# Optimization experiments

Hardware: AMD Instinct MI355X
Metric: run time of the kernel (lower is better)

The kernel has to match this reference:

```python
import jax, jax.numpy as jnp
import numpy as np

N_NODES = 50000
N_EDGES = 1600000
IN_F = 256
OUT_F = 128
ALPHA = 0.2  # LeakyReLU negative slope
EPS = 1e-9


def setup_inputs() -> dict:
    key = jax.random.key(0)
    k1, k2, k3, k4 = jax.random.split(key, 4)
    x = jax.random.normal(k1, (N_NODES, IN_F), dtype=jnp.float32)
    edge_index = jax.random.randint(k2, (2, N_EDGES), 0, N_NODES, dtype=jnp.int64)
    # xavier_uniform-ish scale for params
    W = jax.random.normal(k3, (IN_F, OUT_F), dtype=jnp.float32) * (1.414 / np.sqrt(IN_F + OUT_F))
    a = jax.random.normal(k4, (1, 2 * OUT_F), dtype=jnp.float32) * (1.414 / np.sqrt(1 + 2 * OUT_F))
    return {"x": x, "edge_index": edge_index, "W": W, "a": a}


def reference(x, edge_index, W, a):
    N = x.shape[0]
    F = W.shape[1]
    h = x @ W                                  # [N, F]
    src = edge_index[0]                        # row indices (aggregation target)
    dst = edge_index[1]                        # col indices (neighbor source)
    a_src = a[0, :F]                           # split a.mm(cat(h_src, h_dst).T)
    a_dst = a[0, F:]
    score = h[src] @ a_src + h[dst] @ a_dst    # [E]
    e = jnp.exp(-jax.nn.leaky_relu(score, negative_slope=ALPHA))  # [E]
    # e_rowsum = A @ ones : sum of edge values per row
    rowsum = jax.ops.segment_sum(e, src, num_segments=N)          # [N]
    # h_prime = A @ h : weighted neighbor aggregation per row
    agg = jax.ops.segment_sum(e[:, None] * h[dst], src, num_segments=N)  # [N, F]
    h_prime = agg / (rowsum[:, None] + EPS)
    return jax.nn.elu(h_prime)  # concat=True -> elu
```

## Files before the change

kernel.cpp:

```cpp
#include <hip/hip_runtime.h>
#include <hip/hip_bf16.h>
#include <math.h>

#define N_NODES 50000
#define N_EDGES 1600000
#define IN_F 256
#define OUT_F 128
#define ALPHA 0.2f
#define EPS 1e-9f

#define NPB 32
#define BINS 1563
#define SUBCAP 1536
#define MAXDEG 128
#define PTILE 8192
#define PGRID ((N_EDGES + PTILE - 1) / PTILE)

typedef __attribute__((ext_vector_type(8))) short short8v;
typedef __attribute__((ext_vector_type(4))) float f32x4;

__device__ __forceinline__ unsigned short bf16r(float f) {
  unsigned u = __float_as_uint(f);
  u = (u + 0x7FFFu + ((u >> 16) & 1u)) >> 16;
  return (unsigned short)u;
}

__global__ __launch_bounds__(256) void wcvt_k(const float* __restrict__ W,
                                              unsigned short* __restrict__ Wt) {
  int col = blockIdx.x;
  int k = threadIdx.x;
  Wt[col * IN_F + k] = bf16r(W[(size_t)k * OUT_F + col]);
}

__global__ __launch_bounds__(256) void gemm_mfma(const float* __restrict__ x,
                                                 const unsigned short* __restrict__ Wt,
                                                 const float* __restrict__ a,
                                                 unsigned short* __restrict__ hbs,
                                                 float* __restrict__ s1,
                                                 float* __restrict__ s2) {
  __shared__ float s1p[128], s2p[128];
  const int t = threadIdx.x;
  const int lane = t & 63;
  const int wv = t >> 6;
  const int row0 = blockIdx.x * 128;
  const int wcol0 = wv * 32;
  const int lrow = lane & 15;
  const int lk = (lane >> 4) * 8;

  for (int i = t; i < 128; i += 256) { s1p[i] = 0.f; s2p[i] = 0.f; }

  short8v b[2][8];
#pragma unroll
  for (int cg = 0; cg < 2; ++cg) {
    int col = wcol0 + cg * 16 + lrow;
#pragma unroll
    for (int ks = 0; ks < 8; ++ks)
      b[cg][ks] = *reinterpret_cast<const short8v*>(&Wt[col * IN_F + ks * 32 + lk]);
  }
  const float a1 = a[wcol0 + lrow];
  const float a1b = a[wcol0 + 16 + lrow];
  const float a2 = a[128 + wcol0 + lrow];
  const float a2b = a[128 + wcol0 + 16 + lrow];
  __syncthreads();

  for (int rg = 0; rg < 8; ++rg) {
    int row = row0 + rg * 16 + lrow;
    int rowc = row < N_NODES ? row : N_NODES - 1;
    const float* xr = &x[(size_t)rowc * IN_F];
    short8v av[8];
#pragma unroll
    for (int ks = 0; ks < 8; ++ks) {
      float4 u = *reinterpret_cast<const float4*>(&xr[ks * 32 + lk]);
      float4 v = *reinterpret_cast<const float4*>(&xr[ks * 32 + lk + 4]);
      short8v w;
      w[0] = (short)bf16r(u.x); w[1] = (short)bf16r(u.y);
      w[2] = (short)bf16r(u.z); w[3] = (short)bf16r(u.w);
      w[4] = (short)bf16r(v.x); w[5] = (short)bf16r(v.y);
      w[6] = (short)bf16r(v.z); w[7] = (short)bf16r(v.w);
      av[ks] = w;
    }
    f32x4 acc0 = {0.f, 0.f, 0.f, 0.f};
    f32x4 acc1 = {0.f, 0.f, 0.f, 0.f};
#pragma unroll
    for (int ks = 0; ks < 8; ++ks) {
      acc0 = __builtin_amdgcn_mfma_f32_16x16x32_bf16(av[ks], b[0][ks], acc0, 0, 0, 0);
      acc1 = __builtin_amdgcn_mfma_f32_16x16x32_bf16(av[ks], b[1][ks], acc1, 0, 0, 0);
    }
    int srow0 = row0 + rg * 16 + (lane >> 4) * 4;
#pragma unroll
    for (int r = 0; r < 4; ++r) {
      int srow = srow0 + r;
      if (srow < N_NODES) {
        hbs[(size_t)srow * OUT_F + wcol0 + lrow] = bf16r(acc0[r]);
        hbs[(size_t)srow * OUT_F + wcol0 + 16 + lrow] = bf16r(acc1[r]);
      }
      float p1 = acc0[r] * a1 + acc1[r] * a1b;
      float p2 = acc0[r] * a2 + acc1[r] * a2b;
#pragma unroll
      for (int m = 8; m >= 1; m >>= 1) {
        p1 += __shfl_xor(p1, m, 64);
        p2 += __shfl_xor(p2, m, 64);
      }
      if (lrow == 0) {
        int lr = rg * 16 + (lane >> 4) * 4 + r;
        atomicAdd(&s1p[lr], p1);
        atomicAdd(&s2p[lr], p2);
      }
    }
  }
  __syncthreads();
  for (int i = t; i < 128; i += 256) {
    int g = row0 + i;
    if (g < N_NODES) { s1[g] = s1p[i]; s2[g] = s2p[i]; }
  }
}

__device__ __forceinline__ int load_idx(const int* __restrict__ ei32, int isI64,
                                        long long pos) {
  if (isI64) return (int)(reinterpret_cast<const long long*>(ei32)[pos]);
  return ei32[pos];
}

__global__ __launch_bounds__(512) void part_k(const int* __restrict__ ei,
                                              unsigned* __restrict__ bins,
                                              int* __restrict__ bincur) {
  __shared__ int hist[BINS], cur[BINS], gbase[BINS];
  __shared__ int sf64;
  const int t = threadIdx.x;
  if (t < 64) {
    int nz = 0;
#pragma unroll
    for (int j = 0; j < 4; ++j) nz |= ei[2 * (t + j * 64) + 1];
    unsigned long long any = __ballot(nz != 0);
    if (t == 0) sf64 = (any == 0ull) ? 1 : 0;
  }
  for (int i = t; i < BINS; i += 512) hist[i] = 0;
  __syncthreads();
  const int f64 = sf64;
  const int base = blockIdx.x * PTILE;
  unsigned rec[16];
#pragma unroll
  for (int j = 0; j < 16; ++j) {
    int e = base + j * 512 + t;
    if (e < N_EDGES) {
      unsigned s = (unsigned)load_idx(ei, f64, e);
      unsigned d = (unsigned)load_idx(ei, f64, (long long)N_EDGES + e);
      rec[j] = (s << 16) | d;
      atomicAdd(&hist[s >> 5], 1);
    } else rec[j] = 0xFFFFFFFFu;
  }
  __syncthreads();
  for (int i = t; i < BINS; i += 512) {
    gbase[i] = hist[i] ? atomicAdd(&bincur[i], hist[i]) : 0;
    cur[i] = 0;
  }
  __syncthreads();
#pragma unroll
  for (int j = 0; j < 16; ++j) {
    if (rec[j] != 0xFFFFFFFFu) {
      int bb = rec[j] >> 21;
      int pos = atomicAdd(&cur[bb], 1);
      int o = gbase[bb] + pos;
      if (o < SUBCAP) bins[(size_t)bb * SUBCAP + o] = rec[j];
    }
  }
}

__global__ __launch_bounds__(512) void aggc_k(const unsigned* __restrict__ bins,
                                              const int* __restrict__ bincur,
                                              const float* __restrict__ s1,
                                              const float* __restrict__ s2,
                                              const unsigned* __restrict__ hb,
                                              float* __restrict__ out) {
  __shared__ unsigned sorted[SUBCAP];
  __shared__ uint2 ebuf[8][MAXDEG];
  __shared__ int hist[NPB], cur[NPB], rowptr[NPB + 1];
  const int t = threadIdx.x;
  const int b = blockIdx.x;
  const int lo = b * NPB;
  const int n_b = min(bincur[b], SUBCAP);
  const unsigned* bp = bins + (size_t)b * SUBCAP;

  if (t < NPB) hist[t] = 0;
  __syncthreads();
  unsigned rec[3];
#pragma unroll
  for (int r = 0; r < 3; ++r) {
    int i = t + r * 512;
    rec[r] = 0xFFFFFFFFu;
    if (i < n_b) {
      rec[r] = bp[i];
      atomicAdd(&hist[(rec[r] >> 16) & (NPB - 1)], 1);
    }
  }
  __syncthreads();
  if (t < NPB) {
    int c = hist[t];
    int incl = c;
#pragma unroll
    for (int off = 1; off < NPB; off <<= 1) {
      int v = __shfl_up(incl, off, 64);
      if (t >= off) incl += v;
    }
    rowptr[t + 1] = incl;
    cur[t] = incl - c;
    if (t == 0) rowptr[0] = 0;
  }
  __syncthreads();
#pragma unroll
  for (int r = 0; r < 3; ++r) {
    if (rec[r] != 0xFFFFFFFFu) {
      int sl = (rec[r] >> 16) & (NPB - 1);
      int pos = atomicAdd(&cur[sl], 1);
      sorted[pos] = rec[r] & 0xFFFFu;
    }
  }
  __syncthreads();

  const int wv = t >> 6, lane = t & 63;
  for (int i = 0; i < 4; ++i) {
    int nl = wv * 4 + i;
    int g = lo + nl;
    if (g >= N_NODES) continue;
    int rp = rowptr[nl];
    int cn = min(rowptr[nl + 1] - rp, MAXDEG);
    float s1u = s1[g];
    float rsl = 0.f;
    for (int j = lane; j < cn; j += 64) {
      unsigned d = sorted[rp + j];
      float sc = s1u + s2[d];
      float w = __expf(-fmaxf(sc, ALPHA * sc));
      ebuf[wv][j] = make_uint2(d << 6, __float_as_uint(w));
      rsl += w;
    }
#pragma unroll
    for (int m = 32; m >= 1; m >>= 1) rsl += __shfl_xor(rsl, m, 64);
    float accx = 0.f, accy = 0.f;
    int j = 0;
    for (; j + 7 < cn; j += 8) {
      uint4 e0 = *reinterpret_cast<const uint4*>(&ebuf[wv][j]);
      uint4 e1 = *reinterpret_cast<const uint4*>(&ebuf[wv][j + 2]);
      uint4 e2 = *reinterpret_cast<const uint4*>(&ebuf[wv][j + 4]);
      uint4 e3 = *reinterpret_cast<const uint4*>(&ebuf[wv][j + 6]);
      unsigned v0 = hb[e0.x | lane];
      unsigned v1 = hb[e0.z | lane];
      unsigned v2 = hb[e1.x | lane];
      unsigned v3 = hb[e1.z | lane];
      unsigned v4 = hb[e2.x | lane];
      unsigned v5 = hb[e2.z | lane];
      unsigned v6 = hb[e3.x | lane];
      unsigned v7 = hb[e3.z | lane];
      float w0 = __uint_as_float(e0.y), w1 = __uint_as_float(e0.w);
      float w2 = __uint_as_float(e1.y), w3 = __uint_as_float(e1.w);
      float w4 = __uint_as_float(e2.y), w5 = __uint_as_float(e2.w);
      float w6 = __uint_as_float(e3.y), w7 = __uint_as_float(e3.w);
      accx = fmaf(w0, __uint_as_float(v0 << 16), accx);
      accy = fmaf(w0, __uint_as_float(v0 & 0xFFFF0000u), accy);
      accx = fmaf(w1, __uint_as_float(v1 << 16), accx);
      accy = fmaf(w1, __uint_as_float(v1 & 0xFFFF0000u), accy);
      accx = fmaf(w2, __uint_as_float(v2 << 16), accx);
      accy = fmaf(w2, __uint_as_float(v2 & 0xFFFF0000u), accy);
      accx = fmaf(w3, __uint_as_float(v3 << 16), accx);
      accy = fmaf(w3, __uint_as_float(v3 & 0xFFFF0000u), accy);
      accx = fmaf(w4, __uint_as_float(v4 << 16), accx);
      accy = fmaf(w4, __uint_as_float(v4 & 0xFFFF0000u), accy);
      accx = fmaf(w5, __uint_as_float(v5 << 16), accx);
      accy = fmaf(w5, __uint_as_float(v5 & 0xFFFF0000u), accy);
      accx = fmaf(w6, __uint_as_float(v6 << 16), accx);
      accy = fmaf(w6, __uint_as_float(v6 & 0xFFFF0000u), accy);
      accx = fmaf(w7, __uint_as_float(v7 << 16), accx);
      accy = fmaf(w7, __uint_as_float(v7 & 0xFFFF0000u), accy);
    }
    for (; j < cn; ++j) {
      uint2 e = ebuf[wv][j];
      unsigned v0 = hb[e.x | lane];
      float w0 = __uint_as_float(e.y);
      accx = fmaf(w0, __uint_as_float(v0 << 16), accx);
      accy = fmaf(w0, __uint_as_float(v0 & 0xFFFF0000u), accy);
    }
    float inv = 1.0f / (rsl + EPS);
    float px = accx * inv, py = accy * inv;
    px = px > 0.f ? px : expm1f(px);
    py = py > 0.f ? py : expm1f(py);
    float2 o = {px, py};
    *reinterpret_cast<float2*>(&out[(size_t)g * OUT_F + 2 * lane]) = o;
  }
}

extern "C" void kernel_launch(void* const* d_in, const int* in_sizes, int n_in,
                              void* d_out, int out_size, void* d_ws, size_t ws_size,
                              hipStream_t stream) {
  const float* x = (const float*)d_in[0];
  const int* ei = (const int*)d_in[1];
  const float* W = (const float*)d_in[2];
  const float* a = (const float*)d_in[3];
  float* out = (float*)d_out;

  unsigned* hb = (unsigned*)d_ws;
  float* s1 = (float*)(hb + (size_t)N_NODES * 64);
  float* s2 = s1 + N_NODES;
  int* bincur = (int*)(s2 + N_NODES);
  unsigned* bins = (unsigned*)(bincur + BINS);
  unsigned short* Wt = (unsigned short*)(bins + (size_t)BINS * SUBCAP);

  hipMemsetAsync(bincur, 0, (size_t)BINS * sizeof(int), stream);

  wcvt_k<<<OUT_F, IN_F, 0, stream>>>(W, Wt);
  gemm_mfma<<<(N_NODES + 127) / 128, 256, 0, stream>>>(x, Wt, a, (unsigned short*)hb, s1, s2);
  part_k<<<PGRID, 512, 0, stream>>>(ei, bins, bincur);
  aggc_k<<<BINS, 512, 0, stream>>>(bins, bincur, s1, s2, hb, out);
}
```

Before: 128.9 us.

## Use buffer loads for gather, cheaper bf16 packing, larger partition tiles

The neighbor-feature gather in the aggregation kernel now goes through raw buffer loads with byte offsets when the builtin is available, falling back to plain pointer loads otherwise. The fp32-to-bf16 packing in the GEMM uses a simpler round-half-up pack of two values per word instead of per-element round-to-nearest-even. The partition kernel handles twice as many edges per block, halving the grid, and the in-LDS sorted neighbor list shrinks to 16-bit entries. Together these aim to cut address arithmetic, ALU work, launch blocks and LDS footprint, at the cost of slightly different rounding, more registers in the partition kernel and fewer partition blocks in flight.

```diff
diff --git a/kernel.cpp b/kernel.cpp
--- a/kernel.cpp
+++ b/kernel.cpp
@@ -13,16 +13,28 @@
 #define BINS 1563
 #define SUBCAP 1536
 #define MAXDEG 128
-#define PTILE 8192
+#define PTILE 16384
 #define PGRID ((N_EDGES + PTILE - 1) / PTILE)
 
 typedef __attribute__((ext_vector_type(8))) short short8v;
 typedef __attribute__((ext_vector_type(4))) float f32x4;
+
+#if defined(__has_builtin)
+#if __has_builtin(__builtin_amdgcn_raw_buffer_load_b32) && __has_builtin(__builtin_amdgcn_make_buffer_rsrc)
+#define HAVE_RAWBUF 1
+#endif
+#endif
 
 __device__ __forceinline__ unsigned short bf16r(float f) {
   unsigned u = __float_as_uint(f);
   u = (u + 0x7FFFu + ((u >> 16) & 1u)) >> 16;
   return (unsigned short)u;
+}
+
+__device__ __forceinline__ unsigned pk2(float a, float b) {
+  unsigned ua = (__float_as_uint(a) + 0x8000u) >> 16;
+  unsigned ub = (__float_as_uint(b) + 0x8000u) & 0xFFFF0000u;
+  return ua | ub;
 }
 
 __global__ __launch_bounds__(256) void wcvt_k(const float* __restrict__ W,
@@ -72,12 +84,12 @@
     for (int ks = 0; ks < 8; ++ks) {
       float4 u = *reinterpret_cast<const float4*>(&xr[ks * 32 + lk]);
       float4 v = *reinterpret_cast<const float4*>(&xr[ks * 32 + lk + 4]);
-      short8v w;
-      w[0] = (short)bf16r(u.x); w[1] = (short)bf16r(u.y);
-      w[2] = (short)bf16r(u.z); w[3] = (short)bf16r(u.w);
-      w[4] = (short)bf16r(v.x); w[5] = (short)bf16r(v.y);
-      w[6] = (short)bf16r(v.z); w[7] = (short)bf16r(v.w);
-      av[ks] = w;
+      union { short8v s; unsigned u[4]; } cv;
+      cv.u[0] = pk2(u.x, u.y);
+      cv.u[1] = pk2(u.z, u.w);
+      cv.u[2] = pk2(v.x, v.y);
+      cv.u[3] = pk2(v.z, v.w);
+      av[ks] = cv.s;
     }
     f32x4 acc0 = {0.f, 0.f, 0.f, 0.f};
     f32x4 acc1 = {0.f, 0.f, 0.f, 0.f};
@@ -138,9 +150,9 @@
   __syncthreads();
   const int f64 = sf64;
   const int base = blockIdx.x * PTILE;
-  unsigned rec[16];
-#pragma unroll
-  for (int j = 0; j < 16; ++j) {
+  unsigned rec[32];
+#pragma unroll
+  for (int j = 0; j < 32; ++j) {
     int e = base + j * 512 + t;
     if (e < N_EDGES) {
       unsigned s = (unsigned)load_idx(ei, f64, e);
@@ -156,7 +168,7 @@
   }
   __syncthreads();
 #pragma unroll
-  for (int j = 0; j < 16; ++j) {
+  for (int j = 0; j < 32; ++j) {
     if (rec[j] != 0xFFFFFFFFu) {
       int bb = rec[j] >> 21;
       int pos = atomicAdd(&cur[bb], 1);
@@ -172,7 +184,7 @@
                                               const float* __restrict__ s2,
                                               const unsigned* __restrict__ hb,
                                               float* __restrict__ out) {
-  __shared__ unsigned sorted[SUBCAP];
+  __shared__ unsigned short sorted[SUBCAP];
   __shared__ uint2 ebuf[8][MAXDEG];
   __shared__ int hist[NPB], cur[NPB], rowptr[NPB + 1];
   const int t = threadIdx.x;
@@ -212,12 +224,22 @@
     if (rec[r] != 0xFFFFFFFFu) {
       int sl = (rec[r] >> 16) & (NPB - 1);
       int pos = atomicAdd(&cur[sl], 1);
-      sorted[pos] = rec[r] & 0xFFFFu;
-    }
-  }
-  __syncthreads();
+      sorted[pos] = (unsigned short)(rec[r] & 0xFFFFu);
+    }
+  }
+  __syncthreads();
+
+#ifdef HAVE_RAWBUF
+  __amdgpu_buffer_rsrc_t srsrc = __builtin_amdgcn_make_buffer_rsrc(
+      (void*)hb, (short)0, (int)(N_NODES * OUT_F * 2), 0x00020000);
+#define GATHER(off) ((unsigned)__builtin_amdgcn_raw_buffer_load_b32(srsrc, (int)(off), 0, 0))
+#else
+  const char* hb8 = (const char*)hb;
+#define GATHER(off) (*(const unsigned*)(hb8 + (off)))
+#endif
 
   const int wv = t >> 6, lane = t & 63;
+  const unsigned lane4 = (unsigned)lane << 2;
   for (int i = 0; i < 4; ++i) {
     int nl = wv * 4 + i;
     int g = lo + nl;
@@ -230,7 +252,7 @@
       unsigned d = sorted[rp + j];
       float sc = s1u + s2[d];
       float w = __expf(-fmaxf(sc, ALPHA * sc));
-      ebuf[wv][j] = make_uint2(d << 6, __float_as_uint(w));
+      ebuf[wv][j] = make_uint2(d << 8, __float_as_uint(w));
       rsl += w;
     }
 #pragma unroll
@@ -242,14 +264,14 @@
       uint4 e1 = *reinterpret_cast<const uint4*>(&ebuf[wv][j + 2]);
       uint4 e2 = *reinterpret_cast<const uint4*>(&ebuf[wv][j + 4]);
       uint4 e3 = *reinterpret_cast<const uint4*>(&ebuf[wv][j + 6]);
-      unsigned v0 = hb[e0.x | lane];
-      unsigned v1 = hb[e0.z | lane];
-      unsigned v2 = hb[e1.x | lane];
-      unsigned v3 = hb[e1.z | lane];
-      unsigned v4 = hb[e2.x | lane];
-      unsigned v5 = hb[e2.z | lane];
-      unsigned v6 = hb[e3.x | lane];
-      unsigned v7 = hb[e3.z | lane];
+      unsigned v0 = GATHER(e0.x | lane4);
+      unsigned v1 = GATHER(e0.z | lane4);
+      unsigned v2 = GATHER(e1.x | lane4);
+      unsigned v3 = GATHER(e1.z | lane4);
+      unsigned v4 = GATHER(e2.x | lane4);
+      unsigned v5 = GATHER(e2.z | lane4);
+      unsigned v6 = GATHER(e3.x | lane4);
+      unsigned v7 = GATHER(e3.z | lane4);
       float w0 = __uint_as_float(e0.y), w1 = __uint_as_float(e0.w);
       float w2 = __uint_as_float(e1.y), w3 = __uint_as_float(e1.w);
       float w4 = __uint_as_float(e2.y), w5 = __uint_as_float(e2.w);
@@ -273,7 +295,7 @@
     }
     for (; j < cn; ++j) {
       uint2 e = ebuf[wv][j];
-      unsigned v0 = hb[e.x | lane];
+      unsigned v0 = GATHER(e.x | lane4);
       float w0 = __uint_as_float(e.y);
       accx = fmaf(w0, __uint_as_float(v0 << 16), accx);
       accy = fmaf(w0, __uint_as_float(v0 & 0xFFFF0000u), accy);
@@ -285,6 +307,7 @@
     float2 o = {px, py};
     *reinterpret_cast<float2*>(&out[(size_t)g * OUT_F + 2 * lane]) = o;
   }
+#undef GATHER
 }
 
 extern "C" void kernel_launch(void* const* d_in, const int* in_sizes, int n_in,
```

Result: slower. 140.7 us (+9.2%).
